# Performance work log

Hardware: AMD Instinct MI355X
Metric: run time of the kernel (lower is better)

## Reference

```python
import jax, jax.numpy as jnp
import numpy as np
from jax import lax

B, C_IN, C_OUT, H, W = 32, 96, 96, 56, 56
E = 8          # num_experts
HID = 576      # round(96 * 6)
K = 3          # depthwise kernel size


def setup_inputs() -> dict:
    key = jax.random.key(0)
    ks = jax.random.split(key, 12)
    f = lambda k, s, sc=0.05: jax.random.normal(k, s, dtype=jnp.float32) * sc
    return {
        "x": jax.random.normal(ks[0], (B, C_IN, H, W), dtype=jnp.float32),
        # router for expand conv (input = x, C_IN channels)
        "w_r1": f(ks[1], (E, C_IN)), "b_r1": jnp.zeros((E,), jnp.float32),
        # expert bank for 1x1 expand: [E, HID, C_IN]
        "w1": f(ks[2], (E, HID, C_IN)),
        "g1": jnp.ones((HID,), jnp.float32), "bt1": jnp.zeros((HID,), jnp.float32),
        "m1": f(ks[3], (HID,), 0.01), "v1": jax.random.uniform(ks[4], (HID,), dtype=jnp.float32) + 0.5,
        # router for depthwise conv (input = expanded features, HID channels)
        "w_r2": f(ks[5], (E, HID)), "b_r2": jnp.zeros((E,), jnp.float32),
        # expert bank for depthwise 3x3: [E, HID, K, K] (in/groups = 1)
        "w2": f(ks[6], (E, HID, K, K)),
        "g2": jnp.ones((HID,), jnp.float32), "bt2": jnp.zeros((HID,), jnp.float32),
        "m2": f(ks[7], (HID,), 0.01), "v2": jax.random.uniform(ks[8], (HID,), dtype=jnp.float32) + 0.5,
        # expert bank for 1x1 project: [E, C_OUT, HID]
        "w3": f(ks[9], (E, C_OUT, HID)),
        "g3": jnp.ones((C_OUT,), jnp.float32), "bt3": jnp.zeros((C_OUT,), jnp.float32),
        "m3": f(ks[10], (C_OUT,), 0.01), "v3": jax.random.uniform(ks[11], (C_OUT,), dtype=jnp.float32) + 0.5,
        # block-level router (input = x, C_IN channels) gating the project conv
        "w_r3": f(jax.random.fold_in(key, 99), (E, C_IN)), "b_r3": jnp.zeros((E,), jnp.float32),
    }


def _route(feat, Wf, bf):
    # BasicRouter: global avg pool -> Linear -> sigmoid. feat: [B, C, H, W] -> [B, E]
    return jax.nn.sigmoid(feat.mean(axis=(2, 3)) @ Wf.T + bf)


def _bn(y, g, b, m, v, eps=1e-5):
    inv = g * lax.rsqrt(v + eps)
    return y * inv[None, :, None, None] + (b - m * inv)[None, :, None, None]


def reference(x, w_r1, b_r1, w1, g1, bt1, m1, v1,
              w_r2, b_r2, w2, g2, bt2, m2, v2,
              w3, g3, bt3, m3, v3, w_r3, b_r3):
    r1 = _route(x, w_r1, b_r1)      # [B, E] gate for expand conv
    r_blk = _route(x, w_r3, b_r3)   # [B, E] block router gates project conv

    # --- CondConv 1x1 expand: per-sample mixed kernel as batched GEMM ---
    w1c = jnp.einsum('be,eoc->boc', r1, w1)              # [B, HID, C_IN]
    y = jnp.einsum('bchw,boc->bohw', x, w1c)             # [B, HID, H, W]
    y = jnp.clip(_bn(y, g1, bt1, m1, v1), 0.0, 6.0)      # ReLU6

    # --- CondConv depthwise 3x3 (groups = HID), router on expanded feats ---
    r2 = _route(y, w_r2, b_r2)                           # [B, E]
    kw = jnp.einsum('be,eckl->bckl', r2, w2).reshape(B * HID, 1, K, K)
    y = lax.conv_general_dilated(
        y.reshape(1, B * HID, H, W), kw, (1, 1), 'SAME',
        dimension_numbers=('NCHW', 'OIHW', 'NCHW'),
        feature_group_count=B * HID).reshape(B, HID, H, W)
    y = jnp.clip(_bn(y, g2, bt2, m2, v2), 0.0, 6.0)

    # --- CondConv 1x1 project, gated by the block router(x) ---
    w3c = jnp.einsum('be,eoc->boc', r_blk, w3)           # [B, C_OUT, HID]
    y = jnp.einsum('bchw,boc->bohw', y, w3c)             # [B, C_OUT, H, W]
    y = _bn(y, g3, bt3, m3, v3)

    return x + y  # stride==1 and inp==oup -> residual connection
```

## Files before the change

### kernel.cpp

```cpp
#include <hip/hip_runtime.h>
#include <hip/hip_bf16.h>

#define B_   32
#define CIN  96
#define COUT 96
#define NP   3136
#define NE   8
#define HIDD 576

typedef short bf16x8 __attribute__((ext_vector_type(8)));
typedef float f32x4 __attribute__((ext_vector_type(4)));

__device__ __forceinline__ unsigned short f2bf(float f) {
  __hip_bfloat16 h = __float2bfloat16(f);
  unsigned short u; __builtin_memcpy(&u, &h, 2); return u;
}
__device__ __forceinline__ float bf2f(unsigned short u) {
  unsigned int v = ((unsigned int)u) << 16;
  float f; __builtin_memcpy(&f, &v, 4); return f;
}

__global__ __launch_bounds__(256) void k_transpose(const float* __restrict__ x,
                                                   unsigned short* __restrict__ xt,
                                                   float* __restrict__ xmean) {
  __shared__ float tile[CIN][65];
  int bi = blockIdx.x; int b = bi / 49, pt = bi % 49; int p0 = pt * 64;
  int t = threadIdx.x;
  for (int j = t; j < CIN * 64; j += 256) {
    int c = j >> 6, pi = j & 63;
    tile[c][pi] = x[((size_t)(b * CIN + c)) * NP + p0 + pi];
  }
  __syncthreads();
  if (t < CIN) {
    float s = 0.f;
    for (int i = 0; i < 64; ++i) s += tile[t][i];
    atomicAdd(xmean + b * CIN + t, s);
  }
  for (int j = t; j < 64 * CIN; j += 256) {
    int p = j / CIN, c = j % CIN;
    xt[((size_t)(b * NP + p0 + p)) * CIN + c] = f2bf(tile[c][p]);
  }
}

__global__ __launch_bounds__(64) void k_router1(const float* __restrict__ xmean,
    const float* __restrict__ wr1, const float* __restrict__ br1,
    const float* __restrict__ wr3, const float* __restrict__ br3,
    float* __restrict__ r1, float* __restrict__ rblk) {
  int bi = blockIdx.x; int lane = threadIdx.x;
  const float* wr; const float* br; float* dst; int id;
  if (bi < 256) { wr = wr1; br = br1; dst = r1;   id = bi; }
  else          { wr = wr3; br = br3; dst = rblk; id = bi - 256; }
  int b = id >> 3, e = id & 7;
  float s = 0.f;
  for (int c = lane; c < CIN; c += 64)
    s += xmean[b * CIN + c] * (1.0f / NP) * wr[e * CIN + c];
  s += __shfl_xor(s, 1);  s += __shfl_xor(s, 2);  s += __shfl_xor(s, 4);
  s += __shfl_xor(s, 8);  s += __shfl_xor(s, 16); s += __shfl_xor(s, 32);
  if (lane == 0) dst[id] = 1.0f / (1.0f + __expf(-(s + br[e])));
}

__global__ __launch_bounds__(256) void k_bnprep(
    const float* g1, const float* bt1, const float* m1, const float* v1,
    const float* g2, const float* bt2, const float* m2, const float* v2,
    const float* g3, const float* bt3, const float* m3, const float* v3,
    float* sc1, float* bi1, float* sc2, float* bi2, float* sc3, float* bi3) {
  int i = blockIdx.x * 256 + threadIdx.x;
  if (i < HIDD) {
    float s = g1[i] * rsqrtf(v1[i] + 1e-5f); sc1[i] = s; bi1[i] = bt1[i] - m1[i] * s;
  } else if (i < 2 * HIDD) {
    int c = i - HIDD;
    float s = g2[c] * rsqrtf(v2[c] + 1e-5f); sc2[c] = s; bi2[c] = bt2[c] - m2[c] * s;
  } else if (i < 2 * HIDD + COUT) {
    int c = i - 2 * HIDD;
    float s = g3[c] * rsqrtf(v3[c] + 1e-5f); sc3[c] = s; bi3[c] = bt3[c] - m3[c] * s;
  }
}

__global__ __launch_bounds__(256) void k_mixw(
    const float* __restrict__ w1, const float* __restrict__ r1, unsigned short* __restrict__ w1c,
    const float* __restrict__ w3, const float* __restrict__ rblk, unsigned short* __restrict__ w3c) {
  __shared__ float rsh[256];
  int bi = blockIdx.x; int t = threadIdx.x;
  const float* w; const float* r; unsigned short* dst; int oc0;
  if (bi < 216) { w = w1; r = r1;   dst = w1c; oc0 = bi * 256; }
  else          { w = w3; r = rblk; dst = w3c; oc0 = (bi - 216) * 256; }
  rsh[t] = r[t];
  __syncthreads();
  int oc = oc0 + t;
  float wv[NE];
#pragma unroll
  for (int e = 0; e < NE; ++e) wv[e] = w[(size_t)e * 55296 + oc];
  for (int b = 0; b < B_; ++b) {
    float a = 0.f;
#pragma unroll
    for (int e = 0; e < NE; ++e) a += rsh[b * 8 + e] * wv[e];
    dst[(size_t)b * 55296 + oc] = f2bf(a);
  }
}

__global__ __launch_bounds__(256) void k_expand2(const unsigned short* __restrict__ xt,
    const unsigned short* __restrict__ w1c, const float* __restrict__ sc1,
    const float* __restrict__ bi1, unsigned short* __restrict__ y2,
    float* __restrict__ ysum) {
  __shared__ unsigned short As[64 * 104];
  __shared__ unsigned short Bs[64 * 104];
  int t = threadIdx.x;
  int p0 = blockIdx.x * 64, o0 = blockIdx.y * 64, b = blockIdx.z;
  const unsigned short* ag = w1c + (size_t)b * 55296 + (size_t)o0 * 96;
  const unsigned short* bg = xt + ((size_t)b * NP + p0) * 96;
  for (int j = t; j < 768; j += 256) {
    int r = j / 12, ch = j % 12;
    *(int4*)(As + r * 104 + ch * 8) = *(const int4*)(ag + r * 96 + ch * 8);
    *(int4*)(Bs + r * 104 + ch * 8) = *(const int4*)(bg + r * 96 + ch * 8);
  }
  __syncthreads();
  int lane = t & 63, wv = t >> 6;
  int m = lane & 15, q = lane >> 4;
  f32x4 acc[4];
#pragma unroll
  for (int nt = 0; nt < 4; ++nt) acc[nt] = 0.f;
#pragma unroll
  for (int kk = 0; kk < 3; ++kk) {
    bf16x8 af = *(const bf16x8*)(As + (wv * 16 + m) * 104 + kk * 32 + q * 8);
#pragma unroll
    for (int nt = 0; nt < 4; ++nt) {
      bf16x8 bfb = *(const bf16x8*)(Bs + (nt * 16 + m) * 104 + kk * 32 + q * 8);
      acc[nt] = __builtin_amdgcn_mfma_f32_16x16x32_bf16(af, bfb, acc[nt], 0, 0, 0);
    }
  }
  __syncthreads();
  float sc[4], bb[4];
#pragma unroll
  for (int i = 0; i < 4; ++i) {
    int o = o0 + wv * 16 + q * 4 + i;
    sc[i] = sc1[o]; bb[i] = bi1[o];
  }
  float rs[4] = {0.f, 0.f, 0.f, 0.f};
  unsigned short* T = As;
#pragma unroll
  for (int nt = 0; nt < 4; ++nt) {
    unsigned short pk[4];
#pragma unroll
    for (int i = 0; i < 4; ++i) {
      float v = acc[nt][i] * sc[i] + bb[i];
      v = fminf(fmaxf(v, 0.f), 6.f);
      rs[i] += v;
      pk[i] = f2bf(v);
    }
    uint2 pv; __builtin_memcpy(&pv, pk, 8);
    *(uint2*)(T + (nt * 16 + m) * 72 + wv * 16 + q * 4) = pv;
  }
#pragma unroll
  for (int i = 0; i < 4; ++i) {
    float r = rs[i];
    r += __shfl_xor(r, 1); r += __shfl_xor(r, 2);
    r += __shfl_xor(r, 4); r += __shfl_xor(r, 8);
    if (m == 0) atomicAdd(ysum + b * HIDD + o0 + wv * 16 + q * 4 + i, r);
  }
  __syncthreads();
  for (int j = t; j < 512; j += 256) {
    int r = j >> 3, ch = j & 7;
    *(int4*)(y2 + ((size_t)(b * NP + p0 + r)) * 576 + o0 + ch * 8) =
        *(const int4*)(T + r * 72 + ch * 8);
  }
}

__global__ __launch_bounds__(64) void k_router2(const float* __restrict__ ysum,
    const float* __restrict__ wr2, const float* __restrict__ br2, float* __restrict__ r2) {
  int id = blockIdx.x; int lane = threadIdx.x;
  int b = id >> 3, e = id & 7;
  float s = 0.f;
  for (int h = lane; h < HIDD; h += 64)
    s += ysum[b * HIDD + h] * (1.0f / NP) * wr2[e * HIDD + h];
  s += __shfl_xor(s, 1);  s += __shfl_xor(s, 2);  s += __shfl_xor(s, 4);
  s += __shfl_xor(s, 8);  s += __shfl_xor(s, 16); s += __shfl_xor(s, 32);
  if (lane == 0) r2[id] = 1.0f / (1.0f + __expf(-(s + br2[e])));
}

__global__ __launch_bounds__(256) void k_kwmix2(const float* __restrict__ r2,
    const float* __restrict__ w2, const float* __restrict__ sc2,
    const float* __restrict__ bi2, float* __restrict__ kwt) {
  int i = blockIdx.x * 256 + threadIdx.x;
  if (i >= B_ * HIDD) return;
  int b = i / HIDD, c = i - b * HIDD;
  float rr[NE];
#pragma unroll
  for (int e = 0; e < NE; ++e) rr[e] = r2[b * 8 + e];
  float sc = sc2[c];
  float* dst = kwt + (size_t)b * 5760 + c;
#pragma unroll
  for (int k = 0; k < 9; ++k) {
    float s = 0.f;
#pragma unroll
    for (int e = 0; e < NE; ++e) s += rr[e] * w2[((size_t)e * HIDD + c) * 9 + k];
    dst[k * 576] = s * sc;
  }
  dst[9 * 576] = bi2[c];
}

__global__ __launch_bounds__(192) void k_dwise3(const unsigned short* __restrict__ y2,
    const float* __restrict__ kwt, unsigned short* __restrict__ z2) {
  int h = blockIdx.x, cg = blockIdx.y, b = blockIdx.z;
  int c = cg * 192 + threadIdx.x;
  const float* kp = kwt + (size_t)b * 5760 + c;
  float k0 = kp[0],        k1 = kp[576],      k2 = kp[2 * 576],
        k3 = kp[3 * 576],  k4 = kp[4 * 576],  k5 = kp[5 * 576],
        k6 = kp[6 * 576],  k7 = kp[7 * 576],  k8 = kp[8 * 576],
        bias = kp[9 * 576];
  const unsigned short* base = y2 + ((size_t)(b * NP + h * 56)) * 576 + c;
  unsigned short* zo = z2 + ((size_t)(b * NP + h * 56)) * 576 + c;
  bool hu = h > 0, hd = h < 55;
  float fu = hu ? 1.f : 0.f, fd = hd ? 1.f : 0.f;
  const unsigned short* upr = hu ? (base - 56 * 576) : base;
  const unsigned short* dnr = hd ? (base + 56 * 576) : base;
  float um = 0.f, mm = 0.f, dm = 0.f;
  float uc = bf2f(upr[0]) * fu, mc = bf2f(base[0]), dc = bf2f(dnr[0]) * fd;
  float upc = bf2f(upr[576]) * fu, mpc = bf2f(base[576]), dpc = bf2f(dnr[576]) * fd;
#pragma unroll 8
  for (int w = 0; w < 56; ++w) {
    float un = 0.f, mn = 0.f, dn2 = 0.f;
    if (w < 54) {
      int off = (w + 2) * 576;
      un = bf2f(upr[off]) * fu; mn = bf2f(base[off]); dn2 = bf2f(dnr[off]) * fd;
    }
    float o = um * k0 + uc * k1 + upc * k2
            + mm * k3 + mc * k4 + mpc * k5
            + dm * k6 + dc * k7 + dpc * k8 + bias;
    o = fminf(fmaxf(o, 0.f), 6.f);
    zo[w * 576] = f2bf(o);
    um = uc; uc = upc; upc = un;
    mm = mc; mc = mpc; mpc = mn;
    dm = dc; dc = dpc; dpc = dn2;
  }
}

__global__ __launch_bounds__(384) void k_project3(const unsigned short* __restrict__ z2,
    const unsigned short* __restrict__ w3c, const float* __restrict__ sc3,
    const float* __restrict__ bi3, const float* __restrict__ x, float* __restrict__ out) {
  __shared__ unsigned short As[96 * 72];
  __shared__ unsigned short Bs[64 * 72];
  int t = threadIdx.x;
  int p0 = blockIdx.x * 64, b = blockIdx.z;
  const unsigned short* ag = w3c + (size_t)b * 55296;
  const unsigned short* zb = z2 + ((size_t)(b * NP + p0)) * 576;
  int lane = t & 63, wv = t >> 6;
  int m = lane & 15, q = lane >> 4;
  f32x4 acc[4];
#pragma unroll
  for (int nt = 0; nt < 4; ++nt) acc[nt] = 0.f;
  for (int c0 = 0; c0 < HIDD; c0 += 64) {
    __syncthreads();
    for (int j = t; j < 768; j += 384) {
      int r = j >> 3, ch = j & 7;
      *(int4*)(As + r * 72 + ch * 8) = *(const int4*)(ag + (size_t)r * 576 + c0 + ch * 8);
    }
    for (int j = t; j < 512; j += 384) {
      int r = j >> 3, ch = j & 7;
      *(int4*)(Bs + r * 72 + ch * 8) = *(const int4*)(zb + (size_t)r * 576 + c0 + ch * 8);
    }
    __syncthreads();
#pragma unroll
    for (int kk = 0; kk < 2; ++kk) {
      bf16x8 af = *(const bf16x8*)(As + (wv * 16 + m) * 72 + kk * 32 + q * 8);
#pragma unroll
      for (int nt = 0; nt < 4; ++nt) {
        bf16x8 bfb = *(const bf16x8*)(Bs + (nt * 16 + m) * 72 + kk * 32 + q * 8);
        acc[nt] = __builtin_amdgcn_mfma_f32_16x16x32_bf16(af, bfb, acc[nt], 0, 0, 0);
      }
    }
  }
#pragma unroll
  for (int i = 0; i < 4; ++i) {
    int o = wv * 16 + q * 4 + i;
    float sc = sc3[o], bb = bi3[o];
    size_t base = ((size_t)(b * COUT + o)) * NP + p0;
#pragma unroll
    for (int nt = 0; nt < 4; ++nt) {
      float v = acc[nt][i] * sc + bb + x[base + nt * 16 + m];
      out[base + nt * 16 + m] = v;
    }
  }
}

#define OFF_XT    ((size_t)0)
#define OFF_KWT   OFF_XT
#define OFF_Y     ((size_t)19267584)
#define OFF_Z     ((size_t)134873088)
#define OFF_W1C   ((size_t)250478592)
#define OFF_W3C   ((size_t)254017536)
#define OFF_XMEAN ((size_t)257556480)
#define OFF_YSUM  ((size_t)257568768)
#define OFF_R1    ((size_t)257642496)
#define OFF_RBLK  ((size_t)257643520)
#define OFF_R2    ((size_t)257644544)
#define OFF_SC1   ((size_t)257645568)
#define OFF_BI1   ((size_t)257647872)
#define OFF_SC2   ((size_t)257650176)
#define OFF_BI2   ((size_t)257652480)
#define OFF_SC3   ((size_t)257654784)
#define OFF_BI3   ((size_t)257655168)

extern "C" void kernel_launch(void* const* d_in, const int* in_sizes, int n_in,
                              void* d_out, int out_size, void* d_ws, size_t ws_size,
                              hipStream_t stream) {
  const float* x   = (const float*)d_in[0];
  const float* wr1 = (const float*)d_in[1];
  const float* br1 = (const float*)d_in[2];
  const float* w1  = (const float*)d_in[3];
  const float* g1  = (const float*)d_in[4];
  const float* bt1 = (const float*)d_in[5];
  const float* m1  = (const float*)d_in[6];
  const float* v1  = (const float*)d_in[7];
  const float* wr2 = (const float*)d_in[8];
  const float* br2 = (const float*)d_in[9];
  const float* w2  = (const float*)d_in[10];
  const float* g2  = (const float*)d_in[11];
  const float* bt2 = (const float*)d_in[12];
  const float* m2  = (const float*)d_in[13];
  const float* v2  = (const float*)d_in[14];
  const float* w3  = (const float*)d_in[15];
  const float* g3  = (const float*)d_in[16];
  const float* bt3 = (const float*)d_in[17];
  const float* m3  = (const float*)d_in[18];
  const float* v3  = (const float*)d_in[19];
  const float* wr3 = (const float*)d_in[20];
  const float* br3 = (const float*)d_in[21];
  float* out = (float*)d_out;
  char* ws = (char*)d_ws;

  unsigned short* xt   = (unsigned short*)(ws + OFF_XT);
  unsigned short* y2   = (unsigned short*)(ws + OFF_Y);
  unsigned short* z2   = (unsigned short*)(ws + OFF_Z);
  unsigned short* w1c  = (unsigned short*)(ws + OFF_W1C);
  unsigned short* w3c  = (unsigned short*)(ws + OFF_W3C);
  float* xmean = (float*)(ws + OFF_XMEAN);
  float* ysum  = (float*)(ws + OFF_YSUM);
  float* r1    = (float*)(ws + OFF_R1);
  float* rblk  = (float*)(ws + OFF_RBLK);
  float* r2    = (float*)(ws + OFF_R2);
  float* sc1   = (float*)(ws + OFF_SC1);
  float* bi1   = (float*)(ws + OFF_BI1);
  float* sc2   = (float*)(ws + OFF_SC2);
  float* bi2   = (float*)(ws + OFF_BI2);
  float* sc3   = (float*)(ws + OFF_SC3);
  float* bi3   = (float*)(ws + OFF_BI3);
  float* kwt   = (float*)(ws + OFF_KWT);

  hipMemsetAsync(ws + OFF_XMEAN, 0, 12288 + 73728, stream);

  k_transpose<<<32 * 49, 256, 0, stream>>>(x, xt, xmean);
  k_router1<<<512, 64, 0, stream>>>(xmean, wr1, br1, wr3, br3, r1, rblk);
  k_bnprep<<<5, 256, 0, stream>>>(g1, bt1, m1, v1, g2, bt2, m2, v2, g3, bt3, m3, v3,
                                  sc1, bi1, sc2, bi2, sc3, bi3);
  k_mixw<<<432, 256, 0, stream>>>(w1, r1, w1c, w3, rblk, w3c);
  k_expand2<<<dim3(49, 9, 32), 256, 0, stream>>>(xt, w1c, sc1, bi1, y2, ysum);
  k_router2<<<256, 64, 0, stream>>>(ysum, wr2, br2, r2);
  k_kwmix2<<<72, 256, 0, stream>>>(r2, w2, sc2, bi2, kwt);
  k_dwise3<<<dim3(56, 3, 32), 192, 0, stream>>>(y2, kwt, z2);
  k_project3<<<dim3(49, 1, 32), 384, 0, stream>>>(z2, w3c, sc3, bi3, x, out);
}
```

Baseline: 340.0 us.

## Vectorize depthwise conv over 4 channels and 2 rows, widen project tile

The depthwise 3x3 kernel now has each thread handle 4 channels and 2 output rows. It uses 8-byte vector loads and stores and a rolling 3-column register window, so the shared input rows are reused across both outputs. The project GEMM tile grows from 64 to 112 pixels per block, so each loaded weight tile feeds 7 MFMA column tiles instead of 4. The trade-off is fewer threads and blocks (lower occupancy) and higher register and LDS use per block.

```diff
diff --git a/kernel.cpp b/kernel.cpp
--- a/kernel.cpp
+++ b/kernel.cpp
@@ -17,6 +17,9 @@
 }
 __device__ __forceinline__ float bf2f(unsigned short u) {
   unsigned int v = ((unsigned int)u) << 16;
+  float f; __builtin_memcpy(&f, &v, 4); return f;
+}
+__device__ __forceinline__ float u2f(unsigned int v) {
   float f; __builtin_memcpy(&f, &v, 4); return f;
 }
 
@@ -198,63 +201,104 @@
   dst[9 * 576] = bi2[c];
 }
 
-__global__ __launch_bounds__(192) void k_dwise3(const unsigned short* __restrict__ y2,
+__device__ __forceinline__ f32x4 cvt4(uint2 v) {
+  f32x4 r;
+  r[0] = u2f(v.x << 16); r[1] = u2f(v.x & 0xffff0000u);
+  r[2] = u2f(v.y << 16); r[3] = u2f(v.y & 0xffff0000u);
+  return r;
+}
+__device__ __forceinline__ uint2 pack4(f32x4 v) {
+  uint2 r;
+  r.x = (unsigned)f2bf(v[0]) | ((unsigned)f2bf(v[1]) << 16);
+  r.y = (unsigned)f2bf(v[2]) | ((unsigned)f2bf(v[3]) << 16);
+  return r;
+}
+__device__ __forceinline__ f32x4 clamp6(f32x4 v) {
+#pragma unroll
+  for (int i = 0; i < 4; ++i) v[i] = fminf(fmaxf(v[i], 0.f), 6.f);
+  return v;
+}
+
+__global__ __launch_bounds__(256) void k_dwise4(const unsigned short* __restrict__ y2,
     const float* __restrict__ kwt, unsigned short* __restrict__ z2) {
-  int h = blockIdx.x, cg = blockIdx.y, b = blockIdx.z;
-  int c = cg * 192 + threadIdx.x;
+  int id = blockIdx.x * 256 + threadIdx.x;
+  if (id >= 28 * 144 * 32) return;
+  int cg = id % 144; int rest = id / 144;
+  int hp = rest % 28; int b = rest / 28;
+  int c = cg * 4, h0 = hp * 2;
   const float* kp = kwt + (size_t)b * 5760 + c;
-  float k0 = kp[0],        k1 = kp[576],      k2 = kp[2 * 576],
-        k3 = kp[3 * 576],  k4 = kp[4 * 576],  k5 = kp[5 * 576],
-        k6 = kp[6 * 576],  k7 = kp[7 * 576],  k8 = kp[8 * 576],
-        bias = kp[9 * 576];
-  const unsigned short* base = y2 + ((size_t)(b * NP + h * 56)) * 576 + c;
-  unsigned short* zo = z2 + ((size_t)(b * NP + h * 56)) * 576 + c;
-  bool hu = h > 0, hd = h < 55;
-  float fu = hu ? 1.f : 0.f, fd = hd ? 1.f : 0.f;
-  const unsigned short* upr = hu ? (base - 56 * 576) : base;
-  const unsigned short* dnr = hd ? (base + 56 * 576) : base;
-  float um = 0.f, mm = 0.f, dm = 0.f;
-  float uc = bf2f(upr[0]) * fu, mc = bf2f(base[0]), dc = bf2f(dnr[0]) * fd;
-  float upc = bf2f(upr[576]) * fu, mpc = bf2f(base[576]), dpc = bf2f(dnr[576]) * fd;
-#pragma unroll 8
-  for (int w = 0; w < 56; ++w) {
-    float un = 0.f, mn = 0.f, dn2 = 0.f;
-    if (w < 54) {
-      int off = (w + 2) * 576;
-      un = bf2f(upr[off]) * fu; mn = bf2f(base[off]); dn2 = bf2f(dnr[off]) * fd;
-    }
-    float o = um * k0 + uc * k1 + upc * k2
-            + mm * k3 + mc * k4 + mpc * k5
-            + dm * k6 + dc * k7 + dpc * k8 + bias;
-    o = fminf(fmaxf(o, 0.f), 6.f);
-    zo[w * 576] = f2bf(o);
-    um = uc; uc = upc; upc = un;
-    mm = mc; mc = mpc; mpc = mn;
-    dm = dc; dc = dpc; dpc = dn2;
-  }
-}
-
-__global__ __launch_bounds__(384) void k_project3(const unsigned short* __restrict__ z2,
+  f32x4 tk[9], tb;
+#pragma unroll
+  for (int k = 0; k < 9; ++k) tk[k] = *(const f32x4*)(kp + k * 576);
+  tb = *(const f32x4*)(kp + 9 * 576);
+  bool ok0 = (hp > 0), ok3 = (hp < 27);
+  int r0 = ok0 ? (h0 - 1) : h0;
+  int r3 = ok3 ? (h0 + 2) : (h0 + 1);
+  const unsigned short* rowp[4];
+  rowp[0] = y2 + ((size_t)(b * NP + r0 * 56)) * 576 + c;
+  rowp[1] = y2 + ((size_t)(b * NP + h0 * 56)) * 576 + c;
+  rowp[2] = y2 + ((size_t)(b * NP + (h0 + 1) * 56)) * 576 + c;
+  rowp[3] = y2 + ((size_t)(b * NP + r3 * 56)) * 576 + c;
+  bool rok[4] = {ok0, true, true, ok3};
+  unsigned short* zr0 = z2 + ((size_t)(b * NP + h0 * 56)) * 576 + c;
+  unsigned short* zr1 = zr0 + (size_t)56 * 576;
+
+  f32x4 P[4], C[4], N[4];
+#pragma unroll
+  for (int j = 0; j < 4; ++j) P[j] = 0.f;
+
+#define LOADCOL(D, col) do {                                           \
+    _Pragma("unroll") for (int j = 0; j < 4; ++j) {                    \
+      uint2 raw; raw.x = 0u; raw.y = 0u;                               \
+      if ((col) < 56 && rok[j]) raw = *(const uint2*)(rowp[j] + (size_t)(col) * 576); \
+      D[j] = cvt4(raw);                                                \
+    } } while (0)
+
+#define DSTEP(PP, CC, NN, wcur) do {                                   \
+    f32x4 o0 = tb, o1 = tb;                                            \
+    _Pragma("unroll") for (int jj = 0; jj < 3; ++jj) {                 \
+      o0 += PP[jj] * tk[jj * 3] + CC[jj] * tk[jj * 3 + 1] + NN[jj] * tk[jj * 3 + 2]; \
+      o1 += PP[jj + 1] * tk[jj * 3] + CC[jj + 1] * tk[jj * 3 + 1] + NN[jj + 1] * tk[jj * 3 + 2]; \
+    }                                                                  \
+    *(uint2*)(zr0 + (size_t)(wcur) * 576) = pack4(clamp6(o0));         \
+    *(uint2*)(zr1 + (size_t)(wcur) * 576) = pack4(clamp6(o1));         \
+    LOADCOL(PP, (wcur) + 2);                                           \
+  } while (0)
+
+  LOADCOL(C, 0);
+  LOADCOL(N, 1);
+  for (int w = 0; w < 54; w += 3) {
+    DSTEP(P, C, N, w);
+    DSTEP(C, N, P, w + 1);
+    DSTEP(N, P, C, w + 2);
+  }
+  DSTEP(P, C, N, 54);
+  DSTEP(C, N, P, 55);
+#undef DSTEP
+#undef LOADCOL
+}
+
+__global__ __launch_bounds__(384) void k_project4(const unsigned short* __restrict__ z2,
     const unsigned short* __restrict__ w3c, const float* __restrict__ sc3,
     const float* __restrict__ bi3, const float* __restrict__ x, float* __restrict__ out) {
   __shared__ unsigned short As[96 * 72];
-  __shared__ unsigned short Bs[64 * 72];
+  __shared__ unsigned short Bs[112 * 72];
   int t = threadIdx.x;
-  int p0 = blockIdx.x * 64, b = blockIdx.z;
+  int p0 = blockIdx.x * 112, b = blockIdx.z;
   const unsigned short* ag = w3c + (size_t)b * 55296;
   const unsigned short* zb = z2 + ((size_t)(b * NP + p0)) * 576;
   int lane = t & 63, wv = t >> 6;
   int m = lane & 15, q = lane >> 4;
-  f32x4 acc[4];
-#pragma unroll
-  for (int nt = 0; nt < 4; ++nt) acc[nt] = 0.f;
+  f32x4 acc[7];
+#pragma unroll
+  for (int nt = 0; nt < 7; ++nt) acc[nt] = 0.f;
   for (int c0 = 0; c0 < HIDD; c0 += 64) {
     __syncthreads();
     for (int j = t; j < 768; j += 384) {
       int r = j >> 3, ch = j & 7;
       *(int4*)(As + r * 72 + ch * 8) = *(const int4*)(ag + (size_t)r * 576 + c0 + ch * 8);
     }
-    for (int j = t; j < 512; j += 384) {
+    for (int j = t; j < 896; j += 384) {
       int r = j >> 3, ch = j & 7;
       *(int4*)(Bs + r * 72 + ch * 8) = *(const int4*)(zb + (size_t)r * 576 + c0 + ch * 8);
     }
@@ -263,7 +307,7 @@
     for (int kk = 0; kk < 2; ++kk) {
       bf16x8 af = *(const bf16x8*)(As + (wv * 16 + m) * 72 + kk * 32 + q * 8);
 #pragma unroll
-      for (int nt = 0; nt < 4; ++nt) {
+      for (int nt = 0; nt < 7; ++nt) {
         bf16x8 bfb = *(const bf16x8*)(Bs + (nt * 16 + m) * 72 + kk * 32 + q * 8);
         acc[nt] = __builtin_amdgcn_mfma_f32_16x16x32_bf16(af, bfb, acc[nt], 0, 0, 0);
       }
@@ -275,7 +319,7 @@
     float sc = sc3[o], bb = bi3[o];
     size_t base = ((size_t)(b * COUT + o)) * NP + p0;
 #pragma unroll
-    for (int nt = 0; nt < 4; ++nt) {
+    for (int nt = 0; nt < 7; ++nt) {
       float v = acc[nt][i] * sc + bb + x[base + nt * 16 + m];
       out[base + nt * 16 + m] = v;
     }
@@ -356,6 +400,6 @@
   k_expand2<<<dim3(49, 9, 32), 256, 0, stream>>>(xt, w1c, sc1, bi1, y2, ysum);
   k_router2<<<256, 64, 0, stream>>>(ysum, wr2, br2, r2);
   k_kwmix2<<<72, 256, 0, stream>>>(r2, w2, sc2, bi2, kwt);
-  k_dwise3<<<dim3(56, 3, 32), 192, 0, stream>>>(y2, kwt, z2);
-  k_project3<<<dim3(49, 1, 32), 384, 0, stream>>>(z2, w3c, sc3, bi3, x, out);
-}
+  k_dwise4<<<504, 256, 0, stream>>>(y2, kwt, z2);
+  k_project4<<<dim3(28, 1, 32), 384, 0, stream>>>(z2, w3c, sc3, bi3, x, out);
+}
```

Result: faster. 327.7 us (-3.6%).
